# Optimization experiments

Hardware: AMD Instinct MI355X
Metric: run time of the kernel (lower is better)

Reference implementation:

```python
import jax, jax.numpy as jnp
import numpy as np

N_HEAD = 16
ROPE_BASE = 10000.0


def _rope(x, cos, sin):
    # x: [B,H,T,D]; cos/sin: [T,D/2] broadcast over B,H
    half = x.shape[-1] // 2
    x1, x2 = x[..., :half], x[..., half:]
    return jnp.concatenate([x1 * cos - x2 * sin, x1 * sin + x2 * cos], axis=-1)


def setup_inputs() -> dict:
    key = jax.random.key(0)
    k1, k2, k3 = jax.random.split(key, 3)
    C = 2048
    x = jax.random.normal(k1, (4, 2048, C), dtype=jnp.float32)
    w_qkv = jax.random.normal(k2, (C, 3 * C), dtype=jnp.float32) * 0.02
    w_proj = jax.random.normal(k3, (C, C), dtype=jnp.float32) * 0.02
    return {"x": x, "w_qkv": w_qkv, "w_proj": w_proj}


def reference(x, w_qkv, w_proj):
    B, T, C = x.shape
    H = N_HEAD
    D = C // H
    half = D // 2

    qkv = x @ w_qkv  # [B,T,3C]
    q, k, v = jnp.split(qkv, 3, axis=-1)
    # [B,T,C] -> [B,H,T,D]
    q = q.reshape(B, T, H, D).transpose(0, 2, 1, 3)
    k = k.reshape(B, T, H, D).transpose(0, 2, 1, 3)
    v = v.reshape(B, T, H, D).transpose(0, 2, 1, 3)

    # RoPE cache (start_pos = 0, no kv_cache / prefill path)
    inv_freq = 1.0 / (ROPE_BASE ** (jnp.arange(half, dtype=jnp.float32) / half))
    pos = jnp.arange(T, dtype=jnp.float32)
    freqs = pos[:, None] * inv_freq[None, :]  # [T, half]
    cos, sin = jnp.cos(freqs), jnp.sin(freqs)

    q = _rope(q, cos, sin)
    k = _rope(k, cos, sin)

    # scaled dot-product attention with explicit causal mask
    att = jnp.einsum("bhqd,bhkd->bhqk", q, k) / jnp.sqrt(jnp.asarray(D, x.dtype))
    causal = jnp.arange(T)[:, None] >= jnp.arange(T)[None, :]  # [T,T] bool
    att = jnp.where(causal, att, jnp.asarray(-jnp.inf, att.dtype))
    att = jax.nn.softmax(att, axis=-1)
    # dropout = identity (eval mode)
    out = jnp.einsum("bhqk,bhkd->bhqd", att, v)
    out = out.transpose(0, 2, 1, 3).reshape(B, T, C)
    out = out @ w_proj
    return out, k, v  # (output, new kv-cache)
```

## Files before the change

kernel.cpp:

```cpp
#include <hip/hip_runtime.h>
#include <math.h>

#define CDIM 2048
#define TDIM 2048
#define BDIM 4
#define HDIM 16
#define DDIM 128
#define M1   (BDIM * TDIM)
#define N1   (3 * CDIM)
#define KK   CDIM
#define NT   32

typedef unsigned short u16;
typedef __bf16 bf16x8 __attribute__((ext_vector_type(8)));
typedef float f32x4 __attribute__((ext_vector_type(4)));

__device__ __forceinline__ u16 f2b(float f) {
  union { float f; unsigned u; } x; x.f = f;
  unsigned r = x.u + 0x7fffu + ((x.u >> 16) & 1u);
  return (u16)(r >> 16);
}

__device__ __forceinline__ void gload_lds16(const void* g, void* l) {
  __builtin_amdgcn_global_load_lds(
      (__attribute__((address_space(1))) void*)g,
      (__attribute__((address_space(3))) void*)l, 16, 0, 0);
}

__global__ void convert_x(const float* __restrict__ x, u16* __restrict__ xb, int n4) {
  int i = blockIdx.x * blockDim.x + threadIdx.x;
  if (i < n4) {
    float4 v = ((const float4*)x)[i];
    unsigned long long o = (unsigned long long)f2b(v.x)
                         | ((unsigned long long)f2b(v.y) << 16)
                         | ((unsigned long long)f2b(v.z) << 32)
                         | ((unsigned long long)f2b(v.w) << 48);
    ((unsigned long long*)xb)[i] = o;
  }
}

__global__ void transpose_w(const float* __restrict__ w, u16* __restrict__ wt, int K, int N) {
  __shared__ float tile[32][33];
  const int n0 = blockIdx.x * 32, k0 = blockIdx.y * 32;
  const int tx = threadIdx.x & 31, ty = threadIdx.x >> 5;
  for (int r = ty; r < 32; r += 8)
    tile[r][tx] = w[(k0 + r) * N + n0 + tx];
  __syncthreads();
  for (int r = ty; r < 32; r += 8)
    wt[(n0 + r) * K + k0 + tx] = f2b(tile[tx][r]);
}

__global__ void rope_tab(float* __restrict__ cosT, float* __restrict__ sinT) {
  int i = blockIdx.x * blockDim.x + threadIdx.x;
  int t = i >> 6, d = i & 63;
  double inv = pow(10000.0, -(double)d / 64.0);
  double a = (double)t * inv;
  cosT[i] = (float)cos(a);
  sinT[i] = (float)sin(a);
}

__global__ void transpose_v(const float* __restrict__ v, u16* __restrict__ vt) {
  __shared__ float tile[32][33];
  const int bh = blockIdx.z;
  const int t0 = blockIdx.x * 32, d0 = blockIdx.y * 32;
  const int tx = threadIdx.x & 31, ty = threadIdx.x >> 5;
  const float* src = v + (bh * TDIM + t0) * DDIM + d0;
  for (int r = ty; r < 32; r += 8)
    tile[r][tx] = src[r * DDIM + tx];
  __syncthreads();
  u16* dst = vt + (bh * DDIM + d0) * TDIM + t0;
  for (int r = ty; r < 32; r += 8)
    dst[r * TDIM + tx] = f2b(tile[tx][r]);
}


#define VMW4 asm volatile("s_waitcnt vmcnt(4)" ::: "memory");
#define VMW2 asm volatile("s_waitcnt vmcnt(2)" ::: "memory");
#define VMW0 asm volatile("s_waitcnt vmcnt(0)" ::: "memory");
#define SBAR asm volatile("s_barrier" ::: "memory");
#define NOWAIT

#define GEMM256_TILE(bufA_, bufB_, nA_, nB_, kno_, STG, WMID, WEND)            \
  {                                                                            \
    SBAR    \
    bf16x8 aX[4][2], aY[4][2], bX[2][2], bY[2][2];                             \
                                                     \
    _Pragma("unroll")                                                          \
    for (int i = 0; i < 4; ++i)                                                \
      _Pragma("unroll")                                                        \
      for (int kh = 0; kh < 2; ++kh)                                           \
        aX[i][kh] = *(const bf16x8*)&(bufA_)[aoff + i * 1024 +                 \
                                             (((kh * 4 + quad) ^ rsw) * 8)];   \
    _Pragma("unroll")                                                          \
    for (int j = 0; j < 2; ++j)                                                \
      _Pragma("unroll")                                                        \
      for (int kh = 0; kh < 2; ++kh)                                           \
        bX[j][kh] = *(const bf16x8*)&(bufB_)[boff + j * 1024 +                 \
                                             (((kh * 4 + quad) ^ rsw) * 8)];   \
                                                          \
    __builtin_amdgcn_s_setprio(1);                                             \
    _Pragma("unroll")                                                          \
    for (int i = 0; i < 4; ++i)                                                \
      _Pragma("unroll")                                                        \
      for (int j = 0; j < 2; ++j)                                              \
        _Pragma("unroll")                                                      \
        for (int kh = 0; kh < 2; ++kh)                                         \
          acc[i][j] = __builtin_amdgcn_mfma_f32_16x16x32_bf16(                 \
              aX[i][kh], bX[j][kh], acc[i][j], 0, 0, 0);                       \
    __builtin_amdgcn_s_setprio(0);                                             \
              \
    _Pragma("unroll")                                                          \
    for (int j = 0; j < 2; ++j)                                                \
      _Pragma("unroll")                                                        \
      for (int kh = 0; kh < 2; ++kh)                                           \
        bY[j][kh] = *(const bf16x8*)&(bufB_)[8192 + boff + j * 1024 +          \
                                             (((kh * 4 + quad) ^ rsw) * 8)];   \
    if (STG) {                                                                 \
      _Pragma("unroll")                                                        \
      for (int q = 0; q < 2; ++q)                                              \
        gload_lds16(AgBase + (q * 128) * KK + (kno_), &(nA_)[q * 4096 + ldsw]);\
      _Pragma("unroll")                                                        \
      for (int q = 0; q < 2; ++q)                                              \
        gload_lds16(BgBase + (q * 128) * KK + (kno_),                          \
                    &(nB_)[q * 4096 + ldsw]);                                  \
    }                                                                          \
    WMID                                                                       \
    SBAR                                                \
                                 \
    __builtin_amdgcn_s_setprio(1);                                             \
    _Pragma("unroll")                                                          \
    for (int i = 0; i < 4; ++i)                                                \
      _Pragma("unroll")                                                        \
      for (int j = 0; j < 2; ++j)                                              \
        _Pragma("unroll")                                                      \
        for (int kh = 0; kh < 2; ++kh)                                         \
          acc[i][2 + j] = __builtin_amdgcn_mfma_f32_16x16x32_bf16(             \
              aX[i][kh], bY[j][kh], acc[i][2 + j], 0, 0, 0);                   \
    __builtin_amdgcn_s_setprio(0);                                             \
             \
    _Pragma("unroll")                                                          \
    for (int i = 0; i < 4; ++i)                                                \
      _Pragma("unroll")                                                        \
      for (int kh = 0; kh < 2; ++kh)                                           \
        aY[i][kh] = *(const bf16x8*)&(bufA_)[8192 + aoff + i * 1024 +          \
                                             (((kh * 4 + quad) ^ rsw) * 8)];   \
    if (STG) {                                                                 \
      _Pragma("unroll")                                                        \
      for (int q = 0; q < 2; ++q)                                              \
        gload_lds16(BgBase + (q * 128 + 32) * KK + (kno_),                     \
                    &(nB_)[8192 + q * 4096 + ldsw]);                           \
    }                                                                          \
                                                          \
    __builtin_amdgcn_s_setprio(1);                                             \
    _Pragma("unroll")                                                          \
    for (int i = 0; i < 4; ++i)                                                \
      _Pragma("unroll")                                                        \
      for (int j = 0; j < 2; ++j)                                              \
        _Pragma("unroll")                                                      \
        for (int kh = 0; kh < 2; ++kh)                                         \
          acc[4 + i][2 + j] = __builtin_amdgcn_mfma_f32_16x16x32_bf16(         \
              aY[i][kh], bY[j][kh], acc[4 + i][2 + j], 0, 0, 0);               \
    __builtin_amdgcn_s_setprio(0);                                             \
    if (STG) {                                                                 \
      _Pragma("unroll")                                                        \
      for (int q = 0; q < 2; ++q)                                              \
        gload_lds16(AgBase + (q * 128 + 64) * KK + (kno_),                     \
                    &(nA_)[8192 + q * 4096 + ldsw]);                           \
    }                                                                          \
                    \
    __builtin_amdgcn_s_setprio(1);                                             \
    _Pragma("unroll")                                                          \
    for (int i = 0; i < 4; ++i)                                                \
      _Pragma("unroll")                                                        \
      for (int j = 0; j < 2; ++j)                                              \
        _Pragma("unroll")                                                      \
        for (int kh = 0; kh < 2; ++kh)                                         \
          acc[4 + i][j] = __builtin_amdgcn_mfma_f32_16x16x32_bf16(             \
              aY[i][kh], bX[j][kh], acc[4 + i][j], 0, 0, 0);                   \
    __builtin_amdgcn_s_setprio(0);                                             \
    WEND                                                                       \
  }

#define GEMM256_MAINLOOP(APTR, BPTR)                                           \
  const int rA = lane >> 3, cA = lane & 7;                                     \
  const int w8r = wave * 8 + rA;                                               \
  const int swz8 = (cA ^ rA) * 8;                                              \
  const u16* AgBase = (APTR) + (m0 + w8r) * KK + swz8;                         \
  const int nb = ((w8r >> 5) * 64) + (w8r & 31);                               \
  const u16* BgBase = (BPTR) + (n0 + nb) * KK + swz8;                          \
  const int ldsw = wave * 512;                                                 \
  const int rsw = c16 & 7;                                                     \
  const int aoff = (((wave >> 2) * 64) + c16) * 64;                            \
  const int boff = (((wave & 3) * 32) + c16) * 64;                             \
  f32x4 acc[8][4];                                                             \
  {                                                                            \
    f32x4 z = {0.f, 0.f, 0.f, 0.f};                                            \
    _Pragma("unroll")                                                          \
    for (int i = 0; i < 8; ++i)                                                \
      _Pragma("unroll")                                                        \
      for (int j = 0; j < 4; ++j) acc[i][j] = z;                               \
  }                                                                            \
     \
  _Pragma("unroll")                                                            \
  for (int q = 0; q < 2; ++q)                                                  \
    gload_lds16(AgBase + (q * 128) * KK, &lds[q * 4096 + ldsw]);               \
  _Pragma("unroll")                                                            \
  for (int q = 0; q < 2; ++q)                                                  \
    gload_lds16(BgBase + (q * 128) * KK, &lds[32768 + q * 4096 + ldsw]);       \
  _Pragma("unroll")                                                            \
  for (int q = 0; q < 2; ++q)                                                  \
    gload_lds16(BgBase + (q * 128 + 32) * KK,                                  \
                &lds[32768 + 8192 + q * 4096 + ldsw]);                         \
  _Pragma("unroll")                                                            \
  for (int q = 0; q < 2; ++q)                                                  \
    gload_lds16(AgBase + (q * 128 + 64) * KK, &lds[8192 + q * 4096 + ldsw]);   \
  VMW2                                                                         \
  for (int kt = 0; kt < NT - 1; ++kt) {                                        \
    const int cur = kt & 1;                                                    \
    const u16* bA = &lds[cur * 16384];                                         \
    const u16* bB = &lds[32768 + cur * 16384];                                 \
    u16* nA = &lds[(cur ^ 1) * 16384];                                         \
    u16* nB = &lds[32768 + (cur ^ 1) * 16384];                                 \
    const int kno = (kt + 1) * 64;                                             \
    GEMM256_TILE(bA, bB, nA, nB, kno, 1, VMW4, VMW2)                           \
  }                                                                            \
           \
  GEMM256_TILE((&lds[16384]), (&lds[32768 + 16384]), (&lds[0]),                \
               (&lds[32768]), 0, 0, VMW0, NOWAIT)

__global__ __launch_bounds__(512, 1) void gemm_qkv(
    const u16* __restrict__ A,
    const u16* __restrict__ Bt,
    const float* __restrict__ cosT, const float* __restrict__ sinT,
    u16* __restrict__ qb, u16* __restrict__ kb,
    float* __restrict__ kout, float* __restrict__ vout)
{
  extern __shared__ __align__(16) u16 lds[];
  const int tid = threadIdx.x, wave = tid >> 6, lane = tid & 63;
  const int quad = lane >> 4, c16 = lane & 15;
  const int bid = blockIdx.y * 24 + blockIdx.x;
  const int swz = (bid & 7) * 96 + (bid >> 3);
  const int m0 = (swz / 24) * 256, n0 = (swz % 24) * 256;

  GEMM256_MAINLOOP(A, Bt)

  float* cbuf = (float*)lds;
  const int mat = n0 >> 11;
  const int hbase = (n0 & 2047) >> 7;
  const float qscale = 0.088388347648318447f;
#pragma unroll
  for (int pass = 0; pass < 4; ++pass) {
    __syncthreads();
    if ((wave >> 2) == (pass >> 1)) {
#pragma unroll
      for (int i = 0; i < 4; ++i) {
        const int mf = (pass & 1) * 4 + i;
#pragma unroll
        for (int j = 0; j < 4; ++j)
#pragma unroll
          for (int r = 0; r < 4; ++r)
            cbuf[(i * 16 + quad * 4 + r) * 260 + (wave & 3) * 64 + j * 16 + c16] = acc[mf][j][r];
      }
    }
    __syncthreads();
#pragma unroll
    for (int it = 0; it < 16; ++it) {
      int p = it * 512 + tid;
      int lr = p >> 7;
      int hc = (p >> 6) & 1;
      int d = p & 63;
      float x1 = cbuf[lr * 260 + hc * 128 + d];
      float x2 = cbuf[lr * 260 + hc * 128 + 64 + d];
      int mg = m0 + pass * 64 + lr;
      int b = mg >> 11, t = mg & 2047;
      int h = hbase + hc;
      int idx = ((b * HDIM + h) * TDIM + t) * DDIM + d;
      if (mat == 2) {
        vout[idx] = x1; vout[idx + 64] = x2;
      } else {
        float cs = cosT[t * 64 + d], sn = sinT[t * 64 + d];
        float o1 = x1 * cs - x2 * sn;
        float o2 = x1 * sn + x2 * cs;
        if (mat == 0) {
          qb[idx] = f2b(o1 * qscale); qb[idx + 64] = f2b(o2 * qscale);
        } else {
          kout[idx] = o1; kout[idx + 64] = o2;
          kb[idx] = f2b(o1); kb[idx + 64] = f2b(o2);
        }
      }
    }
  }
}

__global__ __launch_bounds__(512, 1) void gemm_proj(
    const u16* __restrict__ A,
    const u16* __restrict__ Bt,
    float* __restrict__ out)
{
  extern __shared__ __align__(16) u16 lds[];
  const int tid = threadIdx.x, wave = tid >> 6, lane = tid & 63;
  const int quad = lane >> 4, c16 = lane & 15;
  const int bid = blockIdx.y * 8 + blockIdx.x;
  const int swz = (bid & 7) * 32 + (bid >> 3);
  const int m0 = (swz >> 3) * 256, n0 = (swz & 7) * 256;

  GEMM256_MAINLOOP(A, Bt)

  const int wm = (wave >> 2) * 128, wn = (wave & 3) * 64;
#pragma unroll
  for (int mf = 0; mf < 8; ++mf)
#pragma unroll
    for (int nf = 0; nf < 4; ++nf)
#pragma unroll
      for (int r = 0; r < 4; ++r)
        out[(m0 + wm + mf * 16 + quad * 4 + r) * CDIM + n0 + wn + nf * 16 + c16] =
            acc[mf][nf][r];
}

__global__ __launch_bounds__(256, 2) void attn(
    const u16* __restrict__ qb, const u16* __restrict__ kb,
    const u16* __restrict__ vt, u16* __restrict__ att)
{
  __shared__ __attribute__((aligned(16))) u16 sh[24576];
  u16* const ksm = sh;
  u16* const vsm = sh + 8192;
  u16* const psm = sh + 16384;

  const int tid = threadIdx.x, wave = tid >> 6, lane = tid & 63;
  const int quad = lane >> 4, c16 = lane & 15;
  const int bx = blockIdx.x;
  const int bh = blockIdx.y;

  for (int hv = 0; hv < 2; ++hv) {
    const int qt = hv ? (7 - bx) : (bx + 8);
    const int q0 = qt * 128;

    {
      const u16* qg = qb + (bh * TDIM + q0) * DDIM;
      const int rowl = wave * 4 + (lane >> 4);
      const int ch = lane & 15;
#pragma unroll
      for (int r = 0; r < 8; ++r) {
        int row = r * 16 + rowl;
        gload_lds16(qg + row * DDIM + (ch ^ (row & 15)) * 8,
                    &sh[(r * 16 + wave * 4) * 128]);
      }
    }
    __syncthreads();
    bf16x8 qf[2][4];
#pragma unroll
    for (int g = 0; g < 2; ++g)
#pragma unroll
      for (int kp = 0; kp < 4; ++kp)
        qf[g][kp] = *(const bf16x8*)&sh[(g * 64 + wave * 16 + c16) * 128 +
                                        (((kp * 4 + quad) ^ c16) * 8)];
    __syncthreads();

    f32x4 o[2][8];
    f32x4 zero = {0.f, 0.f, 0.f, 0.f};
#pragma unroll
    for (int g = 0; g < 2; ++g)
#pragma unroll
      for (int jd = 0; jd < 8; ++jd) o[g][jd] = zero;
    float mrow[2][4], lrow[2][4];
#pragma unroll
    for (int g = 0; g < 2; ++g)
#pragma unroll
      for (int r = 0; r < 4; ++r) { mrow[g][r] = -INFINITY; lrow[g][r] = 0.f; }

    const int nchunk = 2 * qt + 2;
    for (int kc = 0; kc < nchunk; ++kc) {
      const int kc0 = kc * 64;
      {
        const u16* kg = kb + (bh * TDIM + kc0) * DDIM;
        const int rowl = wave * 4 + (lane >> 4);
        const int ch = lane & 15;
#pragma unroll
        for (int r = 0; r < 4; ++r) {
          int row = r * 16 + rowl;
          gload_lds16(kg + row * DDIM + (ch ^ (row & 15)) * 8,
                      &ksm[(r * 16 + wave * 4) * 128]);
        }
        const u16* vg = vt + bh * (DDIM * TDIM) + kc0;
        const int rowv = wave * 8 + (lane >> 3);
        const int chv = lane & 7;
#pragma unroll
        for (int r = 0; r < 4; ++r) {
          int row = r * 32 + rowv;
          gload_lds16(vg + row * TDIM + (chv ^ (row & 7)) * 8,
                      &vsm[(r * 32 + wave * 8) * 64]);
        }
      }
      __syncthreads();

      f32x4 st[2][4];
#pragma unroll
      for (int g = 0; g < 2; ++g)
#pragma unroll
        for (int j = 0; j < 4; ++j) st[g][j] = zero;
#pragma unroll
      for (int kp = 0; kp < 4; ++kp) {
#pragma unroll
        for (int j = 0; j < 4; ++j) {
          bf16x8 bk = *(const bf16x8*)&ksm[(j * 16 + c16) * 128 +
                                           (((kp * 4 + quad) ^ c16) * 8)];
          st[0][j] = __builtin_amdgcn_mfma_f32_16x16x32_bf16(qf[0][kp], bk, st[0][j], 0, 0, 0);
          st[1][j] = __builtin_amdgcn_mfma_f32_16x16x32_bf16(qf[1][kp], bk, st[1][j], 0, 0, 0);
        }
      }

      u16* const pw = psm + wave * 2048;
      float al2[2][4];
#pragma unroll
      for (int g = 0; g < 2; ++g) {
        const bool dg = (kc >= 2 * qt + g);
        const int qrow_base = q0 + g * 64 + wave * 16 + quad * 4;
#pragma unroll
        for (int r = 0; r < 4; ++r) {
          float mx = -INFINITY;
#pragma unroll
          for (int j = 0; j < 4; ++j) {
            float sv = st[g][j][r];
            if (dg && (kc0 + j * 16 + c16 > qrow_base + r)) sv = -INFINITY;
            st[g][j][r] = sv;
            mx = fmaxf(mx, sv);
          }
          mx = fmaxf(mx, __shfl_xor(mx, 1, 64));
          mx = fmaxf(mx, __shfl_xor(mx, 2, 64));
          mx = fmaxf(mx, __shfl_xor(mx, 4, 64));
          mx = fmaxf(mx, __shfl_xor(mx, 8, 64));
          float mnew = fmaxf(mrow[g][r], mx);
          float al = __expf(mrow[g][r] - mnew);
          mrow[g][r] = mnew;
          al2[g][r] = al;
          float sum = 0.f;
          const int row16 = quad * 4 + r;
#pragma unroll
          for (int j = 0; j < 4; ++j) {
            float p = __expf(st[g][j][r] - mnew);
            sum += p;
            int chunk = (j * 2 + (c16 >> 3)) ^ (row16 & 7);
            pw[g * 1024 + row16 * 64 + chunk * 8 + (c16 & 7)] = f2b(p);
          }
          sum += __shfl_xor(sum, 1, 64);
          sum += __shfl_xor(sum, 2, 64);
          sum += __shfl_xor(sum, 4, 64);
          sum += __shfl_xor(sum, 8, 64);
          lrow[g][r] = lrow[g][r] * al + sum;
        }
#pragma unroll
        for (int jd = 0; jd < 8; ++jd)
#pragma unroll
          for (int r = 0; r < 4; ++r)
            o[g][jd][r] *= al2[g][r];
      }

      asm volatile("s_waitcnt lgkmcnt(0)" ::: "memory");

#pragma unroll
      for (int s = 0; s < 2; ++s) {
        const int chp = ((s * 4 + quad) ^ (c16 & 7)) * 8;
        bf16x8 ap0 = *(const bf16x8*)&pw[c16 * 64 + chp];
        bf16x8 ap1 = *(const bf16x8*)&pw[1024 + c16 * 64 + chp];
#pragma unroll
        for (int jd = 0; jd < 8; ++jd) {
          bf16x8 bv = *(const bf16x8*)&vsm[(jd * 16 + c16) * 64 + chp];
          o[0][jd] = __builtin_amdgcn_mfma_f32_16x16x32_bf16(ap0, bv, o[0][jd], 0, 0, 0);
          o[1][jd] = __builtin_amdgcn_mfma_f32_16x16x32_bf16(ap1, bv, o[1][jd], 0, 0, 0);
        }
      }
      __syncthreads();
    }

    const int b = bh >> 4, h = bh & 15;
#pragma unroll
    for (int g = 0; g < 2; ++g) {
      float ri[4];
#pragma unroll
      for (int r = 0; r < 4; ++r) ri[r] = 1.f / lrow[g][r];
#pragma unroll
      for (int jd = 0; jd < 8; ++jd)
#pragma unroll
        for (int r = 0; r < 4; ++r) {
          int t = q0 + g * 64 + wave * 16 + quad * 4 + r;
          att[(b * TDIM + t) * CDIM + h * DDIM + jd * 16 + c16] = f2b(o[g][jd][r] * ri[r]);
        }
    }
  }
}

extern "C" void kernel_launch(void* const* d_in, const int* in_sizes, int n_in,
                              void* d_out, int out_size, void* d_ws, size_t ws_size,
                              hipStream_t stream) {
  (void)in_sizes; (void)n_in; (void)out_size; (void)ws_size;
  const float* x      = (const float*)d_in[0];
  const float* w_qkv  = (const float*)d_in[1];
  const float* w_proj = (const float*)d_in[2];
  float* out  = (float*)d_out;
  float* kout = out + 16777216;
  float* vout = out + 2 * 16777216;

  char* ws = (char*)d_ws;
  u16*   xb     = (u16*)(ws);
  u16*   wqkvT  = (u16*)(ws + 33554432);
  u16*   wprojT = (u16*)(ws + 58720256);
  float* cosT   = (float*)(ws + 67108864);
  float* sinT   = (float*)(ws + 67633152);
  u16*   qb     = (u16*)(ws + 68157440);
  u16*   kb     = (u16*)(ws + 101711872);
  u16*   vt     = (u16*)(ws + 135266304);
  u16*   att    = xb;

  static int attr_set = 0;
  if (!attr_set) {
    hipFuncSetAttribute((const void*)gemm_qkv,
                        hipFuncAttributeMaxDynamicSharedMemorySize, 131072);
    hipFuncSetAttribute((const void*)gemm_proj,
                        hipFuncAttributeMaxDynamicSharedMemorySize, 131072);
    attr_set = 1;
  }

  convert_x<<<16384, 256, 0, stream>>>(x, xb, 4194304);
  transpose_w<<<dim3(192, 64), 256, 0, stream>>>(w_qkv, wqkvT, KK, N1);
  transpose_w<<<dim3(64, 64), 256, 0, stream>>>(w_proj, wprojT, KK, CDIM);
  rope_tab<<<512, 256, 0, stream>>>(cosT, sinT);
  gemm_qkv<<<dim3(24, 32), 512, 131072, stream>>>(xb, wqkvT, cosT, sinT, qb, kb, kout, vout);
  transpose_v<<<dim3(64, 4, 64), 256, 0, stream>>>(vout, vt);
  attn<<<dim3(8, 64), 256, 0, stream>>>(qb, kb, vt, att);
  gemm_proj<<<dim3(8, 32), 512, 131072, stream>>>(att, wprojT, out);
}
```

Before: 768.9 us.

## Restructure GEMM main loop into finer-grained quarter-tile stages with deeper prefetch

```diff
diff --git a/kernel.cpp b/kernel.cpp
--- a/kernel.cpp
+++ b/kernel.cpp
@@ -74,111 +74,76 @@
 }
 
 
-#define VMW4 asm volatile("s_waitcnt vmcnt(4)" ::: "memory");
-#define VMW2 asm volatile("s_waitcnt vmcnt(2)" ::: "memory");
+#define VMW6 asm volatile("s_waitcnt vmcnt(6)" ::: "memory");
 #define VMW0 asm volatile("s_waitcnt vmcnt(0)" ::: "memory");
 #define SBAR asm volatile("s_barrier" ::: "memory");
+#define LGKM0 asm volatile("s_waitcnt lgkmcnt(0)" ::: "memory");
+#define SCHB  __builtin_amdgcn_sched_barrier(0);
 #define NOWAIT
 
-#define GEMM256_TILE(bufA_, bufB_, nA_, nB_, kno_, STG, WMID, WEND)            \
-  {                                                                            \
-    SBAR    \
-    bf16x8 aX[4][2], aY[4][2], bX[2][2], bY[2][2];                             \
-                                                     \
+#define READ_A(dst, base)                                                      \
+  _Pragma("unroll")                                                            \
+  for (int i = 0; i < 4; ++i)                                                  \
     _Pragma("unroll")                                                          \
-    for (int i = 0; i < 4; ++i)                                                \
-      _Pragma("unroll")                                                        \
-      for (int kh = 0; kh < 2; ++kh)                                           \
-        aX[i][kh] = *(const bf16x8*)&(bufA_)[aoff + i * 1024 +                 \
-                                             (((kh * 4 + quad) ^ rsw) * 8)];   \
+    for (int kh = 0; kh < 2; ++kh)                                             \
+      dst[i][kh] = *(const bf16x8*)&(base)[aoff + i * 1024 +                   \
+                                           (((kh * 4 + quad) ^ rsw) * 8)];
+
+#define READ_B(dst, base)                                                      \
+  _Pragma("unroll")                                                            \
+  for (int j = 0; j < 2; ++j)                                                  \
     _Pragma("unroll")                                                          \
-    for (int j = 0; j < 2; ++j)                                                \
-      _Pragma("unroll")                                                        \
-      for (int kh = 0; kh < 2; ++kh)                                           \
-        bX[j][kh] = *(const bf16x8*)&(bufB_)[boff + j * 1024 +                 \
-                                             (((kh * 4 + quad) ^ rsw) * 8)];   \
-                                                          \
-    __builtin_amdgcn_s_setprio(1);                                             \
+    for (int kh = 0; kh < 2; ++kh)                                             \
+      dst[j][kh] = *(const bf16x8*)&(base)[boff + j * 1024 +                   \
+                                           (((kh * 4 + quad) ^ rsw) * 8)];
+
+#define MFMA16(mi, nj, AFR, BFR)                                               \
+  __builtin_amdgcn_s_setprio(1);                                               \
+  _Pragma("unroll")                                                            \
+  for (int kh = 0; kh < 2; ++kh)                                               \
     _Pragma("unroll")                                                          \
     for (int i = 0; i < 4; ++i)                                                \
       _Pragma("unroll")                                                        \
       for (int j = 0; j < 2; ++j)                                              \
-        _Pragma("unroll")                                                      \
-        for (int kh = 0; kh < 2; ++kh)                                         \
-          acc[i][j] = __builtin_amdgcn_mfma_f32_16x16x32_bf16(                 \
-              aX[i][kh], bX[j][kh], acc[i][j], 0, 0, 0);                       \
-    __builtin_amdgcn_s_setprio(0);                                             \
-              \
-    _Pragma("unroll")                                                          \
-    for (int j = 0; j < 2; ++j)                                                \
-      _Pragma("unroll")                                                        \
-      for (int kh = 0; kh < 2; ++kh)                                           \
-        bY[j][kh] = *(const bf16x8*)&(bufB_)[8192 + boff + j * 1024 +          \
-                                             (((kh * 4 + quad) ^ rsw) * 8)];   \
-    if (STG) {                                                                 \
-      _Pragma("unroll")                                                        \
-      for (int q = 0; q < 2; ++q)                                              \
-        gload_lds16(AgBase + (q * 128) * KK + (kno_), &(nA_)[q * 4096 + ldsw]);\
-      _Pragma("unroll")                                                        \
-      for (int q = 0; q < 2; ++q)                                              \
-        gload_lds16(BgBase + (q * 128) * KK + (kno_),                          \
-                    &(nB_)[q * 4096 + ldsw]);                                  \
-    }                                                                          \
-    WMID                                                                       \
-    SBAR                                                \
-                                 \
-    __builtin_amdgcn_s_setprio(1);                                             \
-    _Pragma("unroll")                                                          \
-    for (int i = 0; i < 4; ++i)                                                \
-      _Pragma("unroll")                                                        \
-      for (int j = 0; j < 2; ++j)                                              \
-        _Pragma("unroll")                                                      \
-        for (int kh = 0; kh < 2; ++kh)                                         \
-          acc[i][2 + j] = __builtin_amdgcn_mfma_f32_16x16x32_bf16(             \
-              aX[i][kh], bY[j][kh], acc[i][2 + j], 0, 0, 0);                   \
-    __builtin_amdgcn_s_setprio(0);                                             \
+        acc[(mi) + i][(nj) + j] = __builtin_amdgcn_mfma_f32_16x16x32_bf16(     \
+            AFR[i][kh], BFR[j][kh], acc[(mi) + i][(nj) + j], 0, 0, 0);         \
+  __builtin_amdgcn_s_setprio(0);
+
+#define STG2(gbase, extra, k, dst)                                             \
+  _Pragma("unroll")                                                            \
+  for (int q = 0; q < 2; ++q)                                                  \
+    gload_lds16((gbase) + (q * 128 + (extra)) * KK + (k),                      \
+                &(dst)[q * 4096 + ldsw]);
+
+#define HALF_ITER(AX, BX, BYlo, kt1, kt2, S1, S2, W4)                          \
+  {                                                                            \
+    bf16x8 aF[4][2], bL[2][2], bH[2][2];                                       \
+                                                   \
+    READ_A(aF, (AX))                                                           \
+    READ_B(bL, (BX))                                                           \
+    if (S1) { STG2(BgBase, 0, (kt1), (BYlo)) }                                 \
+    SBAR LGKM0 SCHB                                                            \
+    MFMA16(0, 0, aF, bL)                                                       \
+    SBAR                                                                       \
+          \
+    READ_B(bH, (BX) + 8192)                                                    \
+    if (S2) { STG2(AgBase, 0, (kt2), (AX)) }                                   \
+    SBAR LGKM0 SCHB                                                            \
+    MFMA16(0, 2, aF, bH)                                                       \
+    SBAR                                                                       \
+                                  \
+    READ_A(aF, (AX) + 8192)                                                    \
+    if (S2) { STG2(BgBase, 32, (kt2), (BX) + 8192) }                           \
+    SBAR LGKM0 SCHB                                                            \
+    MFMA16(4, 2, aF, bH)                                                       \
+    SBAR                                                                       \
              \
-    _Pragma("unroll")                                                          \
-    for (int i = 0; i < 4; ++i)                                                \
-      _Pragma("unroll")                                                        \
-      for (int kh = 0; kh < 2; ++kh)                                           \
-        aY[i][kh] = *(const bf16x8*)&(bufA_)[8192 + aoff + i * 1024 +          \
-                                             (((kh * 4 + quad) ^ rsw) * 8)];   \
-    if (STG) {                                                                 \
-      _Pragma("unroll")                                                        \
-      for (int q = 0; q < 2; ++q)                                              \
-        gload_lds16(BgBase + (q * 128 + 32) * KK + (kno_),                     \
-                    &(nB_)[8192 + q * 4096 + ldsw]);                           \
-    }                                                                          \
-                                                          \
-    __builtin_amdgcn_s_setprio(1);                                             \
-    _Pragma("unroll")                                                          \
-    for (int i = 0; i < 4; ++i)                                                \
-      _Pragma("unroll")                                                        \
-      for (int j = 0; j < 2; ++j)                                              \
-        _Pragma("unroll")                                                      \
-        for (int kh = 0; kh < 2; ++kh)                                         \
-          acc[4 + i][2 + j] = __builtin_amdgcn_mfma_f32_16x16x32_bf16(         \
-              aY[i][kh], bY[j][kh], acc[4 + i][2 + j], 0, 0, 0);               \
-    __builtin_amdgcn_s_setprio(0);                                             \
-    if (STG) {                                                                 \
-      _Pragma("unroll")                                                        \
-      for (int q = 0; q < 2; ++q)                                              \
-        gload_lds16(AgBase + (q * 128 + 64) * KK + (kno_),                     \
-                    &(nA_)[8192 + q * 4096 + ldsw]);                           \
-    }                                                                          \
-                    \
-    __builtin_amdgcn_s_setprio(1);                                             \
-    _Pragma("unroll")                                                          \
-    for (int i = 0; i < 4; ++i)                                                \
-      _Pragma("unroll")                                                        \
-      for (int j = 0; j < 2; ++j)                                              \
-        _Pragma("unroll")                                                      \
-        for (int kh = 0; kh < 2; ++kh)                                         \
-          acc[4 + i][j] = __builtin_amdgcn_mfma_f32_16x16x32_bf16(             \
-              aY[i][kh], bX[j][kh], acc[4 + i][j], 0, 0, 0);                   \
-    __builtin_amdgcn_s_setprio(0);                                             \
-    WEND                                                                       \
+    READ_B(bL, (BX))                                                           \
+    if (S2) { STG2(AgBase, 64, (kt2), (AX) + 8192) }                           \
+    SBAR LGKM0 SCHB                                                            \
+    MFMA16(4, 0, aF, bL)                                                       \
+    W4                                                                         \
+    SBAR                                                                       \
   }
 
 #define GEMM256_MAINLOOP(APTR, BPTR)                                           \
@@ -200,33 +165,25 @@
       _Pragma("unroll")                                                        \
       for (int j = 0; j < 4; ++j) acc[i][j] = z;                               \
   }                                                                            \
-     \
-  _Pragma("unroll")                                                            \
-  for (int q = 0; q < 2; ++q)                                                  \
-    gload_lds16(AgBase + (q * 128) * KK, &lds[q * 4096 + ldsw]);               \
-  _Pragma("unroll")                                                            \
-  for (int q = 0; q < 2; ++q)                                                  \
-    gload_lds16(BgBase + (q * 128) * KK, &lds[32768 + q * 4096 + ldsw]);       \
-  _Pragma("unroll")                                                            \
-  for (int q = 0; q < 2; ++q)                                                  \
-    gload_lds16(BgBase + (q * 128 + 32) * KK,                                  \
-                &lds[32768 + 8192 + q * 4096 + ldsw]);                         \
-  _Pragma("unroll")                                                            \
-  for (int q = 0; q < 2; ++q)                                                  \
-    gload_lds16(AgBase + (q * 128 + 64) * KK, &lds[8192 + q * 4096 + ldsw]);   \
-  VMW2                                                                         \
-  for (int kt = 0; kt < NT - 1; ++kt) {                                        \
-    const int cur = kt & 1;                                                    \
-    const u16* bA = &lds[cur * 16384];                                         \
-    const u16* bB = &lds[32768 + cur * 16384];                                 \
-    u16* nA = &lds[(cur ^ 1) * 16384];                                         \
-    u16* nB = &lds[32768 + (cur ^ 1) * 16384];                                 \
-    const int kno = (kt + 1) * 64;                                             \
-    GEMM256_TILE(bA, bB, nA, nB, kno, 1, VMW4, VMW2)                           \
+      \
+  STG2(AgBase, 0, 0, (&lds[0]))                                                \
+  STG2(BgBase, 0, 0, (&lds[32768]))                                            \
+  STG2(BgBase, 32, 0, (&lds[40960]))                                           \
+  STG2(AgBase, 64, 0, (&lds[8192]))                                            \
+  STG2(AgBase, 0, 64, (&lds[16384]))                                           \
+  STG2(BgBase, 32, 64, (&lds[57344]))                                          \
+  STG2(AgBase, 64, 64, (&lds[24576]))                                          \
+  VMW6                        \
+  SBAR                                                                         \
+  for (int it = 0; it < 15; ++it) {                                            \
+    const int k1 = (2 * it + 1) * 64, k2 = (2 * it + 2) * 64;                  \
+    const int k4 = (2 * it + 3) * 64;                                          \
+    HALF_ITER((&lds[0]), (&lds[32768]), (&lds[49152]), k1, k2, 1, 1, VMW6)     \
+    HALF_ITER((&lds[16384]), (&lds[49152]), (&lds[32768]), k2, k4, 1, 1, VMW6) \
   }                                                                            \
-           \
-  GEMM256_TILE((&lds[16384]), (&lds[32768 + 16384]), (&lds[0]),                \
-               (&lds[32768]), 0, 0, VMW0, NOWAIT)
+          \
+  HALF_ITER((&lds[0]), (&lds[32768]), (&lds[49152]), 31 * 64, 0, 1, 0, VMW0)   \
+  HALF_ITER((&lds[16384]), (&lds[49152]), (&lds[32768]), 0, 0, 0, 0, NOWAIT)
 
 __global__ __launch_bounds__(512, 1) void gemm_qkv(
     const u16* __restrict__ A,
```

Result: no change. 765.9 us (-0.4%).
